# Kernel tuning notes

Hardware: AMD Instinct MI355X
Metric: run time of the kernel (lower is better)

## Reference

```python
import jax, jax.numpy as jnp
import numpy as np

B, A, F, T = 4096, 64, 124, 8
H1, H2 = 64, 16


def setup_inputs() -> dict:
    key = jax.random.key(0)
    ks = jax.random.split(key, 10)
    x = jax.random.normal(ks[0], (B, A, F + 1), dtype=jnp.float32)
    types = jax.random.randint(ks[1], (B, A), 0, T).astype(jnp.float32)
    x = x.at[:, :, 0].set(types)  # column 0 stores atom-type index
    mask = (jax.random.uniform(ks[2], (B, A)) < 0.9).astype(jnp.float32)
    s1 = 1.0 / np.sqrt(F)
    s2 = 1.0 / np.sqrt(H1)
    s3 = 1.0 / np.sqrt(H2)
    return {
        "x_padded": x,
        "mask": mask,
        "W1": jax.random.normal(ks[3], (T, F, H1), dtype=jnp.float32) * s1,
        "b1": jax.random.normal(ks[4], (T, H1), dtype=jnp.float32) * s1,
        "W2": jax.random.normal(ks[5], (T, H1, H2), dtype=jnp.float32) * s2,
        "b2": jax.random.normal(ks[6], (T, H2), dtype=jnp.float32) * s2,
        "W3": jax.random.normal(ks[7], (T, H2, 1), dtype=jnp.float32) * s3,
        "b3": jax.random.normal(ks[8], (T, 1), dtype=jnp.float32) * s3,
    }


def reference(x_padded, mask, W1, b1, W2, b2, W3, b3):
    # x_padded: [B, A, 1+F]; mask: [B, A]
    type_idx = x_padded[:, :, 0].astype(jnp.int32)           # [B, A]
    feats = x_padded[:, :, 1:]                               # [B, A, F]
    n_types = W1.shape[0]
    # Faithful to the original: every type's subnet runs on the FULL batch
    # with non-matching atoms zero-masked (bias paths still contribute).
    type_mask = (type_idx[None, :, :] == jnp.arange(n_types)[:, None, None]).astype(feats.dtype)  # [T,B,A]
    sel = feats[None, :, :, :] * type_mask[..., None]        # [T,B,A,F]
    h = jax.nn.relu(jnp.einsum('tbaf,tfh->tbah', sel, W1) + b1[:, None, None, :])
    h = jax.nn.relu(jnp.einsum('tbah,thg->tbag', h, W2) + b2[:, None, None, :])
    o = jnp.einsum('tbag,tgo->tbao', h, W3) + b3[:, None, None, :]  # [T,B,A,1]
    per_atom = (o[..., 0] * mask[None, :, :]).sum(axis=0)   # [B, A]
    return per_atom.sum(axis=1, keepdims=True)               # [B, 1]
```

## Files before the change

kernel.cpp:

```cpp
#include <hip/hip_runtime.h>
#include <stdint.h>

#define NMOL 4096
#define NATOMS (NMOL * 64)
#define NF 124
#define NT 8
#define ROWV 125
#define CAP 65536

#define WS_DCONST  0
#define WS_CURSOR  64
#define WS_W1S     128
#define WS_W2T     131200
#define WS_LIST    147712

#define HS 72

typedef __attribute__((ext_vector_type(8))) short short8;
typedef __attribute__((ext_vector_type(4))) float floatx4;
typedef __attribute__((ext_vector_type(4), aligned(4))) float floatx4u;
typedef __attribute__((ext_vector_type(4))) unsigned int uint4v;

__device__ __forceinline__ unsigned short f2bf(float f) {
    unsigned u = __builtin_bit_cast(unsigned, f);
    u += 0x7fffu + ((u >> 16) & 1u);
    return (unsigned short)(u >> 16);
}
__device__ __forceinline__ unsigned pk2(float a, float b) {
    return (unsigned)f2bf(a) | ((unsigned)f2bf(b) << 16);
}
__device__ __forceinline__ void ld_lds16(const void* g, void* lds) {
    __builtin_amdgcn_global_load_lds(
        (const __attribute__((address_space(1))) unsigned int*)g,
        (__attribute__((address_space(3))) unsigned int*)lds, 16, 0, 0);
}

__global__ __launch_bounds__(256) void k_setup(const float* __restrict__ W1,
                                               const float* __restrict__ b1,
                                               const float* __restrict__ W2,
                                               const float* __restrict__ b2,
                                               const float* __restrict__ W3,
                                               const float* __restrict__ b3,
                                               float* __restrict__ dconst,
                                               unsigned* __restrict__ cursor,
                                               unsigned short* __restrict__ W1S,
                                               unsigned short* __restrict__ W2T,
                                               float* __restrict__ out) {
    int tid = threadIdx.x, b = blockIdx.x;
    if (b == 0) {
        __shared__ float c[NT];
        if (tid < 128) {
            int t = tid >> 4, g = tid & 15;
            float acc = b2[t * 16 + g];
            for (int h = 0; h < 64; ++h) {
                float h1 = b1[t * 64 + h];
                h1 = h1 > 0.f ? h1 : 0.f;
                acc += h1 * W2[(size_t)t * 1024 + h * 16 + g];
            }
            float h2 = acc > 0.f ? acc : 0.f;
            float v = h2 * W3[t * 16 + g];
            #pragma unroll
            for (int off = 1; off < 16; off <<= 1) v += __shfl_xor(v, off);
            if (g == 0) c[t] = v + b3[t];
        }
        if (tid < NT) cursor[tid] = (unsigned)(tid * CAP);
        __syncthreads();
        if (tid == 0) {
            float T_ = 0.f;
            for (int i = 0; i < NT; ++i) T_ += c[i];
            for (int i = 0; i < NT; ++i) dconst[i] = T_ - c[i] + b3[i];
        }
    } else if (b <= 8) {
        int t = b - 1;
        const float* w1g = W1 + (size_t)t * NF * 64;
        unsigned short* dst = W1S + (size_t)t * 8192;
        for (int id = tid; id < 1024; id += 256) {
            int h = id >> 4, cc = id & 15;
            unsigned u[4];
            #pragma unroll
            for (int j = 0; j < 4; ++j) {
                int f0 = cc * 8 + 2 * j;
                unsigned short lo = (f0 < NF)     ? f2bf(w1g[f0 * 64 + h])       : (unsigned short)0;
                unsigned short hi = (f0 + 1 < NF) ? f2bf(w1g[(f0 + 1) * 64 + h]) : (unsigned short)0;
                u[j] = (unsigned)lo | ((unsigned)hi << 16);
            }
            int p = cc ^ (h & 15);
            *(uint4v*)(dst + h * 128 + p * 8) = (uint4v){u[0], u[1], u[2], u[3]};
        }
        unsigned short* d2 = W2T + (size_t)t * 1024;
        for (int i = tid; i < 1024; i += 256) {
            int g = i >> 6, h = i & 63;
            d2[i] = f2bf(W2[(size_t)t * 1024 + h * 16 + g]);
        }
    } else {
        out[(b - 9) * 256 + tid] = 0.0f;
    }
}

__global__ __launch_bounds__(256) void k_sort(const float* __restrict__ x,
                                              const float* __restrict__ mask,
                                              unsigned* __restrict__ cursor,
                                              unsigned* __restrict__ list) {
    __shared__ unsigned hist[NT], basep[NT], cur[NT];
    int tid = threadIdx.x;
    if (tid < NT) { hist[tid] = 0u; cur[tid] = 0u; }
    __syncthreads();
    int base = blockIdx.x * 1024;
    unsigned char tb[4];
    for (int i = 0; i < 4; ++i) {
        int atom = base + i * 256 + tid;
        float tf = x[(size_t)atom * ROWV];
        float m  = mask[atom];
        tb[i] = 0xFF;
        if (m != 0.0f) { tb[i] = (unsigned char)(int)tf; atomicAdd(&hist[tb[i]], 1u); }
    }
    __syncthreads();
    if (tid < NT && hist[tid]) basep[tid] = atomicAdd(&cursor[tid], hist[tid]);
    __syncthreads();
    for (int i = 0; i < 4; ++i) {
        if (tb[i] != 0xFF) {
            unsigned p = basep[tb[i]] + atomicAdd(&cur[tb[i]], 1u);
            list[p] = (unsigned)(base + i * 256 + tid);
        }
    }
}

__global__ __launch_bounds__(256, 4) void k_mlp(const float* __restrict__ x,
                                                const unsigned short* __restrict__ W1S,
                                                const float* __restrict__ b1,
                                                const unsigned short* __restrict__ W2T,
                                                const float* __restrict__ b2,
                                                const float* __restrict__ W3,
                                                const unsigned* __restrict__ cursor,
                                                const float* __restrict__ dconst,
                                                const unsigned* __restrict__ list,
                                                float* __restrict__ out) {
    __shared__ unsigned short sW[64 * 128];
    __shared__ unsigned short sH[128 * HS];
    __shared__ unsigned sIds[128];

    int t    = blockIdx.x >> 9;
    int tile = blockIdx.x & 511;
    int cnt  = (int)(cursor[t] - (unsigned)(t * CAP));
    int valid = cnt - (tile << 7);
    if (valid <= 0) return;
    if (valid > 128) valid = 128;
    int rowstart = t * CAP + (tile << 7);

    int tid  = threadIdx.x;
    int wv   = tid >> 6;
    int lane = tid & 63;
    int quad = lane >> 4, l15 = lane & 15;
    int rowbase = wv * 32;

    {
        const char* src = (const char*)W1S + (size_t)t * 16384 + wv * 4096 + lane * 16;
        char*       dst = (char*)sW + wv * 4096;
        #pragma unroll
        for (int i = 0; i < 4; ++i) ld_lds16(src + i * 1024, dst + i * 1024);
    }
    if (tid < 128) sIds[tid] = list[rowstart + (tid < valid ? tid : 0)];

    float b1v[4];
    #pragma unroll
    for (int n = 0; n < 4; ++n) b1v[n] = b1[t * 64 + n * 16 + l15];

    __syncthreads();

    short8 afrag[2][4];
    #pragma unroll
    for (int m = 0; m < 2; ++m) {
        unsigned atom = sIds[rowbase + m * 16 + l15];
        const float* rp = x + (size_t)atom * ROWV + 1;
        #pragma unroll
        for (int ks = 0; ks < 4; ++ks) {
            int k0 = ks * 32 + quad * 8;
            floatx4 f0 = (floatx4)(*(const floatx4u*)(rp + k0));
            floatx4 f1 = (floatx4)0.f;
            if (!(ks == 3 && quad == 3))
                f1 = (floatx4)(*(const floatx4u*)(rp + k0 + 4));
            uint4v uu = (uint4v){pk2(f0[0], f0[1]), pk2(f0[2], f0[3]),
                                 pk2(f1[0], f1[1]), pk2(f1[2], f1[3])};
            afrag[m][ks] = __builtin_bit_cast(short8, uu);
        }
    }

    floatx4 c1[2][4];
    #pragma unroll
    for (int m = 0; m < 2; ++m)
        #pragma unroll
        for (int n = 0; n < 4; ++n) c1[m][n] = (floatx4)0.f;

    #pragma unroll
    for (int ks = 0; ks < 4; ++ks) {
        short8 bf[4];
        #pragma unroll
        for (int n = 0; n < 4; ++n)
            bf[n] = *(const short8*)(sW + (n * 16 + l15) * 128 + (((ks * 4 + quad) ^ l15) << 3));
        #pragma unroll
        for (int n = 0; n < 4; ++n) {
            c1[0][n] = __builtin_amdgcn_mfma_f32_16x16x32_bf16(afrag[0][ks], bf[n], c1[0][n], 0, 0, 0);
            c1[1][n] = __builtin_amdgcn_mfma_f32_16x16x32_bf16(afrag[1][ks], bf[n], c1[1][n], 0, 0, 0);
        }
    }

    #pragma unroll
    for (int m = 0; m < 2; ++m)
        #pragma unroll
        for (int n = 0; n < 4; ++n) {
            int col = n * 16 + l15;
            #pragma unroll
            for (int r = 0; r < 4; ++r) {
                float v = c1[m][n][r] + b1v[n];
                v = v > 0.f ? v : 0.f;
                sH[(rowbase + m * 16 + quad * 4 + r) * HS + col] = f2bf(v);
            }
        }

    const unsigned short* w2t = W2T + (size_t)t * 1024;
    floatx4 c2[2];
    c2[0] = (floatx4)0.f; c2[1] = (floatx4)0.f;
    #pragma unroll
    for (int ks = 0; ks < 2; ++ks) {
        int ko = ks * 32 + quad * 8;
        short8 a0 = *(const short8*)(sH + (rowbase + l15) * HS + ko);
        short8 a1 = *(const short8*)(sH + (rowbase + 16 + l15) * HS + ko);
        short8 bw = *(const short8*)(w2t + l15 * 64 + ko);
        c2[0] = __builtin_amdgcn_mfma_f32_16x16x32_bf16(a0, bw, c2[0], 0, 0, 0);
        c2[1] = __builtin_amdgcn_mfma_f32_16x16x32_bf16(a1, bw, c2[1], 0, 0, 0);
    }

    float b2v = b2[t * 16 + l15];
    float w3v = W3[t * 16 + l15];
    float dct = dconst[t];
    #pragma unroll
    for (int m = 0; m < 2; ++m) {
        float h2v[4];
        #pragma unroll
        for (int r = 0; r < 4; ++r) {
            float v = c2[m][r] + b2v;
            v = v > 0.f ? v : 0.f;
            h2v[r] = v * w3v;
        }
        #pragma unroll
        for (int off = 1; off < 16; off <<= 1)
            #pragma unroll
            for (int r = 0; r < 4; ++r) h2v[r] += __shfl_xor(h2v[r], off);
        if (l15 == 0) {
            #pragma unroll
            for (int r = 0; r < 4; ++r) {
                int row = rowbase + m * 16 + quad * 4 + r;
                if (row < valid) {
                    unsigned atom = sIds[row];
                    atomicAdd(&out[atom >> 6], h2v[r] + dct);
                }
            }
        }
    }
}

extern "C" void kernel_launch(void* const* d_in, const int* in_sizes, int n_in,
                              void* d_out, int out_size, void* d_ws, size_t ws_size,
                              hipStream_t stream) {
    const float* x    = (const float*)d_in[0];
    const float* mask = (const float*)d_in[1];
    const float* W1   = (const float*)d_in[2];
    const float* b1   = (const float*)d_in[3];
    const float* W2   = (const float*)d_in[4];
    const float* b2   = (const float*)d_in[5];
    const float* W3   = (const float*)d_in[6];
    const float* b3   = (const float*)d_in[7];
    float* out = (float*)d_out;

    char* ws = (char*)d_ws;
    float*          dconst = (float*)(ws + WS_DCONST);
    unsigned*       cursor = (unsigned*)(ws + WS_CURSOR);
    unsigned short* W1S    = (unsigned short*)(ws + WS_W1S);
    unsigned short* W2T    = (unsigned short*)(ws + WS_W2T);
    unsigned*       list   = (unsigned*)(ws + WS_LIST);

    k_setup<<<25, 256, 0, stream>>>(W1, b1, W2, b2, W3, b3, dconst, cursor, W1S, W2T, out);
    k_sort<<<256, 256, 0, stream>>>(x, mask, cursor, list);
    k_mlp<<<NT * (CAP / 128), 256, 0, stream>>>(x, W1S, b1, W2T, b2, W3,
                                                cursor, dconst, list, out);
}
```

Baseline: 219.1 us.

## Replace LDS atomics in sort with wave ballots; drop LDS id staging in MLP

The sort kernel now ranks atoms inside each wave with ballot/popcount instead of per-atom LDS atomics, does a per-block prefix over wave counts, and launches twice as many blocks with two atoms per thread. The MLP kernel loads atom ids straight from the list into registers instead of staging them in shared memory. It also hoists the W2/b2/W3/dconst loads earlier and moves the barrier after the x gather, so global loads overlap the W1 LDS copy. This removes atomic contention and one barrier-bound dependency, at the cost of extra global reads of the list in the epilogue and more registers.

```diff
diff --git a/kernel.cpp b/kernel.cpp
--- a/kernel.cpp
+++ b/kernel.cpp
@@ -101,26 +101,52 @@
                                               const float* __restrict__ mask,
                                               unsigned* __restrict__ cursor,
                                               unsigned* __restrict__ list) {
-    __shared__ unsigned hist[NT], basep[NT], cur[NT];
+    __shared__ unsigned scnt[2][4][NT];
+    __shared__ unsigned sbase[2][4][NT];
     int tid = threadIdx.x;
-    if (tid < NT) { hist[tid] = 0u; cur[tid] = 0u; }
-    __syncthreads();
-    int base = blockIdx.x * 1024;
-    unsigned char tb[4];
-    for (int i = 0; i < 4; ++i) {
+    int wv = tid >> 6, lane = tid & 63;
+    int base = blockIdx.x * 512;
+
+    int ty_[2];
+    unsigned long long mym[2];
+    #pragma unroll
+    for (int i = 0; i < 2; ++i) {
         int atom = base + i * 256 + tid;
         float tf = x[(size_t)atom * ROWV];
         float m  = mask[atom];
-        tb[i] = 0xFF;
-        if (m != 0.0f) { tb[i] = (unsigned char)(int)tf; atomicAdd(&hist[tb[i]], 1u); }
+        int tt = (m != 0.0f) ? (int)tf : -1;
+        ty_[i] = tt;
+        unsigned long long bm = 0ull;
+        unsigned mycnt = 0;
+        #pragma unroll
+        for (int ty = 0; ty < NT; ++ty) {
+            unsigned long long b = __ballot(tt == ty);
+            if (ty == tt) bm = b;
+            if (lane == ty) mycnt = (unsigned)__popcll(b);
+        }
+        mym[i] = bm;
+        if (lane < NT) scnt[i][wv][lane] = mycnt;
     }
     __syncthreads();
-    if (tid < NT && hist[tid]) basep[tid] = atomicAdd(&cursor[tid], hist[tid]);
+    if (tid < NT) {
+        unsigned tot = 0;
+        #pragma unroll
+        for (int i = 0; i < 2; ++i)
+            #pragma unroll
+            for (int w = 0; w < 4; ++w) tot += scnt[i][w][tid];
+        unsigned run = atomicAdd(&cursor[tid], tot);
+        #pragma unroll
+        for (int i = 0; i < 2; ++i)
+            #pragma unroll
+            for (int w = 0; w < 4; ++w) { sbase[i][w][tid] = run; run += scnt[i][w][tid]; }
+    }
     __syncthreads();
-    for (int i = 0; i < 4; ++i) {
-        if (tb[i] != 0xFF) {
-            unsigned p = basep[tb[i]] + atomicAdd(&cur[tb[i]], 1u);
-            list[p] = (unsigned)(base + i * 256 + tid);
+    #pragma unroll
+    for (int i = 0; i < 2; ++i) {
+        int tt = ty_[i];
+        if (tt >= 0) {
+            unsigned rank = (unsigned)__popcll(mym[i] & ((1ull << lane) - 1ull));
+            list[sbase[i][wv][tt] + rank] = (unsigned)(base + i * 256 + tid);
         }
     }
 }
@@ -137,7 +163,6 @@
                                                 float* __restrict__ out) {
     __shared__ unsigned short sW[64 * 128];
     __shared__ unsigned short sH[128 * HS];
-    __shared__ unsigned sIds[128];
 
     int t    = blockIdx.x >> 9;
     int tile = blockIdx.x & 511;
@@ -159,19 +184,30 @@
         #pragma unroll
         for (int i = 0; i < 4; ++i) ld_lds16(src + i * 1024, dst + i * 1024);
     }
-    if (tid < 128) sIds[tid] = list[rowstart + (tid < valid ? tid : 0)];
+
+    unsigned aid[2];
+    #pragma unroll
+    for (int m = 0; m < 2; ++m) {
+        int row = rowbase + m * 16 + l15;
+        aid[m] = list[rowstart + (row < valid ? row : 0)];
+    }
 
     float b1v[4];
     #pragma unroll
     for (int n = 0; n < 4; ++n) b1v[n] = b1[t * 64 + n * 16 + l15];
-
-    __syncthreads();
+    const unsigned short* w2t = W2T + (size_t)t * 1024;
+    short8 bw2[2];
+    #pragma unroll
+    for (int ks = 0; ks < 2; ++ks)
+        bw2[ks] = *(const short8*)(w2t + l15 * 64 + ks * 32 + quad * 8);
+    float b2v = b2[t * 16 + l15];
+    float w3v = W3[t * 16 + l15];
+    float dct = dconst[t];
 
     short8 afrag[2][4];
     #pragma unroll
     for (int m = 0; m < 2; ++m) {
-        unsigned atom = sIds[rowbase + m * 16 + l15];
-        const float* rp = x + (size_t)atom * ROWV + 1;
+        const float* rp = x + (size_t)aid[m] * ROWV + 1;
         #pragma unroll
         for (int ks = 0; ks < 4; ++ks) {
             int k0 = ks * 32 + quad * 8;
@@ -185,6 +221,8 @@
         }
     }
 
+    __syncthreads();
+
     floatx4 c1[2][4];
     #pragma unroll
     for (int m = 0; m < 2; ++m)
@@ -217,7 +255,6 @@
             }
         }
 
-    const unsigned short* w2t = W2T + (size_t)t * 1024;
     floatx4 c2[2];
     c2[0] = (floatx4)0.f; c2[1] = (floatx4)0.f;
     #pragma unroll
@@ -225,14 +262,10 @@
         int ko = ks * 32 + quad * 8;
         short8 a0 = *(const short8*)(sH + (rowbase + l15) * HS + ko);
         short8 a1 = *(const short8*)(sH + (rowbase + 16 + l15) * HS + ko);
-        short8 bw = *(const short8*)(w2t + l15 * 64 + ko);
-        c2[0] = __builtin_amdgcn_mfma_f32_16x16x32_bf16(a0, bw, c2[0], 0, 0, 0);
-        c2[1] = __builtin_amdgcn_mfma_f32_16x16x32_bf16(a1, bw, c2[1], 0, 0, 0);
-    }
-
-    float b2v = b2[t * 16 + l15];
-    float w3v = W3[t * 16 + l15];
-    float dct = dconst[t];
+        c2[0] = __builtin_amdgcn_mfma_f32_16x16x32_bf16(a0, bw2[ks], c2[0], 0, 0, 0);
+        c2[1] = __builtin_amdgcn_mfma_f32_16x16x32_bf16(a1, bw2[ks], c2[1], 0, 0, 0);
+    }
+
     #pragma unroll
     for (int m = 0; m < 2; ++m) {
         float h2v[4];
@@ -251,7 +284,7 @@
             for (int r = 0; r < 4; ++r) {
                 int row = rowbase + m * 16 + quad * 4 + r;
                 if (row < valid) {
-                    unsigned atom = sIds[row];
+                    unsigned atom = list[rowstart + row];
                     atomicAdd(&out[atom >> 6], h2v[r] + dct);
                 }
             }
@@ -280,7 +313,7 @@
     unsigned*       list   = (unsigned*)(ws + WS_LIST);
 
     k_setup<<<25, 256, 0, stream>>>(W1, b1, W2, b2, W3, b3, dconst, cursor, W1S, W2T, out);
-    k_sort<<<256, 256, 0, stream>>>(x, mask, cursor, list);
+    k_sort<<<512, 256, 0, stream>>>(x, mask, cursor, list);
     k_mlp<<<NT * (CAP / 128), 256, 0, stream>>>(x, W1S, b1, W2T, b2, W3,
                                                 cursor, dconst, list, out);
 }
```

Measured after the change: 224.0 us. 2.2% more time.
